# Optimization experiments

Hardware: AMD Instinct MI355X
Metric: run time of the kernel (lower is better)

## Reference

```python
import jax, jax.numpy as jnp
import numpy as np

N = 50000
E = 800000
D = 64
UNITS = 128


def _linear_params(key, fan_in, fan_out):
    k1, k2 = jax.random.split(key)
    bound = 1.0 / np.sqrt(fan_in)
    W = jax.random.uniform(k1, (fan_in, fan_out), minval=-bound, maxval=bound, dtype=jnp.float32)
    b = jax.random.uniform(k2, (fan_out,), minval=-bound, maxval=bound, dtype=jnp.float32)
    return W, b


def setup_inputs() -> dict:
    key = jax.random.key(0)
    ks = jax.random.split(key, 7)
    x = jax.random.normal(ks[0], (N, D), dtype=jnp.float32)
    edge_tensor = jax.random.randint(ks[1], (2, E), 0, N, dtype=jnp.int64)
    W1, b1 = _linear_params(ks[2], D, 2 * D)
    W2, b2 = _linear_params(ks[3], 2 * D, 4 * D)
    W3, b3 = _linear_params(ks[4], 4 * D, UNITS)
    W4, b4 = _linear_params(ks[5], UNITS, UNITS)
    W5, b5 = _linear_params(ks[6], UNITS, 1)
    return {"x": x, "edge_tensor": edge_tensor,
            "W1": W1, "b1": b1, "W2": W2, "b2": b2, "W3": W3, "b3": b3,
            "W4": W4, "b4": b4, "W5": W5, "b5": b5}


def _gin_conv(h, src, dst, W, b):
    # GINConv with default eps=0: MLP((1+eps)*x_i + sum_{j in N(i)} x_j)
    msgs = h[src]                                    # [E, d] gather
    agg = jax.ops.segment_sum(msgs, dst, num_segments=N)  # [N, d] scatter-add
    return jax.nn.relu((agg + h) @ W + b)


def reference(x, edge_tensor, W1, b1, W2, b2, W3, b3, W4, b4, W5, b5):
    src = edge_tensor[0]
    dst = edge_tensor[1]
    h = _gin_conv(x, src, dst, W1, b1)   # [N, 2D]
    h = _gin_conv(h, src, dst, W2, b2)   # [N, 4D]
    h = jax.nn.relu(h @ W3 + b3)         # [N, units]
    h = jax.nn.relu(h @ W4 + b4)         # [N, units]
    return h @ W5 + b5                   # [N, 1]
```

## Files before the change

kernel.cpp:

```cpp
#include <hip/hip_runtime.h>
#include <cstddef>

#define N_NODES 50000
#define N_EDGES 800000

__global__ void zero_int_kernel(int* __restrict__ p, int n) {
    int stride = gridDim.x * blockDim.x;
    for (int i = blockIdx.x * blockDim.x + threadIdx.x; i < n; i += stride) p[i] = 0;
}

__global__ void hist_kernel(const int* __restrict__ dst, int* __restrict__ deg, int E) {
    int stride = gridDim.x * blockDim.x;
    for (int e = blockIdx.x * blockDim.x + threadIdx.x; e < E; e += stride)
        atomicAdd(&deg[dst[e]], 1);
}

__global__ __launch_bounds__(1024)
void scan_blocks(const int* __restrict__ deg, int* __restrict__ loc,
                 int* __restrict__ part, int n) {
    __shared__ int wsum[16];
    const int lane = threadIdx.x & 63;
    const int wid  = threadIdx.x >> 6;
    int i = blockIdx.x * 1024 + threadIdx.x;
    int v = (i < n) ? deg[i] : 0;
    int s = v;
#pragma unroll
    for (int off = 1; off < 64; off <<= 1) {
        int t = __shfl_up(s, off, 64);
        if (lane >= off) s += t;
    }
    if (lane == 63) wsum[wid] = s;
    __syncthreads();
    if (wid == 0) {
        int ws = (lane < 16) ? wsum[lane] : 0;
#pragma unroll
        for (int off = 1; off < 16; off <<= 1) {
            int t = __shfl_up(ws, off, 64);
            if (lane >= off) ws += t;
        }
        if (lane < 16) wsum[lane] = ws;
    }
    __syncthreads();
    int excl = (wid ? wsum[wid - 1] : 0) + s - v;
    if (i < n) loc[i] = excl;
    if (threadIdx.x == 1023) part[blockIdx.x] = wsum[15];
}

__global__ void scan_tops(int* __restrict__ part, int nb) {
    int lane = threadIdx.x;
    int v = (lane < nb) ? part[lane] : 0;
    int s = v;
#pragma unroll
    for (int off = 1; off < 64; off <<= 1) {
        int t = __shfl_up(s, off, 64);
        if (lane >= off) s += t;
    }
    if (lane < nb) part[lane] = s - v;
    if (lane == nb - 1) part[nb] = s;
}

__global__ __launch_bounds__(1024)
void scan_add(const int* __restrict__ loc, const int* __restrict__ part,
              int* __restrict__ row_ptr, int* __restrict__ cursor, int n, int nb) {
    int i = blockIdx.x * 1024 + threadIdx.x;
    if (i < n) {
        int r = loc[i] + part[i >> 10];
        row_ptr[i] = r;
        cursor[i]  = r;
    }
    if (i == 0) row_ptr[n] = part[nb];
}

__global__ void fill_kernel(const int* __restrict__ src, const int* __restrict__ dst,
                            int* __restrict__ cursor, int* __restrict__ col, int E) {
    int stride = gridDim.x * blockDim.x;
    for (int e = blockIdx.x * blockDim.x + threadIdx.x; e < E; e += stride) {
        int p = atomicAdd(&cursor[dst[e]], 1);
        col[p] = src[e];
    }
}

template<int D>
__global__ __launch_bounds__(256)
void gin_aggregate(const float* __restrict__ feat, const int* __restrict__ row_ptr,
                   const int* __restrict__ col, float* __restrict__ agg, int n) {
    int gwid = (blockIdx.x * blockDim.x + threadIdx.x) >> 6;
    int lane = threadIdx.x & 63;
    int nwav = (gridDim.x * blockDim.x) >> 6;
    for (int v = gwid; v < n; v += nwav) {
        float2 acc;
        if constexpr (D == 128) acc = ((const float2*)(feat + (size_t)v * D))[lane];
        else { acc.x = feat[(size_t)v * D + lane]; acc.y = 0.f; }
        int beg = row_ptr[v], end = row_ptr[v + 1];
        for (int j = beg; j < end; j += 64) {
            int batch = end - j; if (batch > 64) batch = 64;
            int e = (lane < batch) ? col[j + lane] : 0;
            for (int k = 0; k < batch; ++k) {
                int s = __shfl(e, k, 64);
                if constexpr (D == 128) {
                    float2 r = ((const float2*)(feat + (size_t)s * D))[lane];
                    acc.x += r.x; acc.y += r.y;
                } else {
                    acc.x += feat[(size_t)s * D + lane];
                }
            }
        }
        if constexpr (D == 128) ((float2*)(agg + (size_t)v * D))[lane] = acc;
        else agg[(size_t)v * D + lane] = acc.x;
    }
}

template<int BN>
__global__ __launch_bounds__(256)
void gemm_bias_relu(const float* __restrict__ A, const float* __restrict__ W,
                    const float* __restrict__ bias, float* __restrict__ C,
                    int M, int K, int N, int do_relu) {
    constexpr int TN = BN / 16;
    __shared__ __align__(16) float As[16][132];
    __shared__ __align__(16) float Bs[16][BN + 4];

    const int tid = threadIdx.x;
    const int tx  = tid & 15;
    const int ty  = tid >> 4;
    const int row0 = blockIdx.y * 128;
    const int col0 = blockIdx.x * BN;

    float acc[8][TN];
#pragma unroll
    for (int i = 0; i < 8; ++i)
#pragma unroll
        for (int j = 0; j < TN; ++j) acc[i][j] = 0.f;

    constexpr int BF4   = BN / 4;
    constexpr int BLOAD = 16 * BF4 / 256;

    for (int k0 = 0; k0 < K; k0 += 16) {
#pragma unroll
        for (int h = 0; h < 2; ++h) {
            int idx = tid + h * 256;
            int ar  = idx >> 2;
            int akc = (idx & 3) << 2;
            int arow = row0 + ar; if (arow >= M) arow = M - 1;
            float4 av = *(const float4*)(A + (size_t)arow * K + k0 + akc);
            As[akc + 0][ar] = av.x;
            As[akc + 1][ar] = av.y;
            As[akc + 2][ar] = av.z;
            As[akc + 3][ar] = av.w;
        }
#pragma unroll
        for (int h = 0; h < BLOAD; ++h) {
            int idx = tid + h * 256;
            int kr  = idx / BF4;
            int cc  = (idx % BF4) << 2;
            float4 bv = *(const float4*)(W + (size_t)(k0 + kr) * N + col0 + cc);
            *(float4*)(&Bs[kr][cc]) = bv;
        }
        __syncthreads();
#pragma unroll
        for (int kk = 0; kk < 16; ++kk) {
            float a[8];
            float4 a0 = *(const float4*)(&As[kk][ty << 2]);
            float4 a1 = *(const float4*)(&As[kk][64 + (ty << 2)]);
            a[0]=a0.x; a[1]=a0.y; a[2]=a0.z; a[3]=a0.w;
            a[4]=a1.x; a[5]=a1.y; a[6]=a1.z; a[7]=a1.w;
            float b[TN];
            float4 b0 = *(const float4*)(&Bs[kk][tx << 2]);
            b[0]=b0.x; b[1]=b0.y; b[2]=b0.z; b[3]=b0.w;
            if constexpr (TN == 8) {
                float4 b1 = *(const float4*)(&Bs[kk][64 + (tx << 2)]);
                b[4]=b1.x; b[5]=b1.y; b[6]=b1.z; b[7]=b1.w;
            }
#pragma unroll
            for (int i = 0; i < 8; ++i)
#pragma unroll
                for (int j = 0; j < TN; ++j)
                    acc[i][j] = fmaf(a[i], b[j], acc[i][j]);
        }
        __syncthreads();
    }

    float bs[TN];
    {
        float4 bb0 = *(const float4*)(bias + col0 + (tx << 2));
        bs[0]=bb0.x; bs[1]=bb0.y; bs[2]=bb0.z; bs[3]=bb0.w;
        if constexpr (TN == 8) {
            float4 bb1 = *(const float4*)(bias + col0 + 64 + (tx << 2));
            bs[4]=bb1.x; bs[5]=bb1.y; bs[6]=bb1.z; bs[7]=bb1.w;
        }
    }
#pragma unroll
    for (int i = 0; i < 8; ++i) {
        int row = row0 + ((i < 4) ? (ty << 2) + i : 64 + (ty << 2) + (i - 4));
        if (row < M) {
#pragma unroll
            for (int g = 0; g < TN / 4; ++g) {
                float4 v;
                float* vp = &v.x;
#pragma unroll
                for (int j = 0; j < 4; ++j) {
                    float t = acc[i][g * 4 + j] + bs[g * 4 + j];
                    if (do_relu) t = fmaxf(t, 0.f);
                    vp[j] = t;
                }
                *(float4*)(C + (size_t)row * N + col0 + g * 64 + (tx << 2)) = v;
            }
        }
    }
}

__global__ void out_proj_kernel(const float* __restrict__ h, const float* __restrict__ w,
                                const float* __restrict__ b, float* __restrict__ out, int M) {
    int lane = threadIdx.x & 63;
    int wave = threadIdx.x >> 6;
    int wpb  = blockDim.x >> 6;
    float w0 = w[lane], w1 = w[64 + lane];
    float bb = b[0];
    for (int row = blockIdx.x * wpb + wave; row < M; row += gridDim.x * wpb) {
        const float* hr = h + (size_t)row * 128;
        float s = hr[lane] * w0 + hr[64 + lane] * w1;
#pragma unroll
        for (int off = 32; off > 0; off >>= 1) s += __shfl_xor(s, off, 64);
        if (lane == 0) out[row] = s + bb;
    }
}

extern "C" void kernel_launch(void* const* d_in, const int* in_sizes, int n_in,
                              void* d_out, int out_size, void* d_ws, size_t ws_size,
                              hipStream_t stream) {
    const float* x    = (const float*)d_in[0];
    const int*   edge = (const int*)d_in[1];
    const float* W1 = (const float*)d_in[2];
    const float* b1 = (const float*)d_in[3];
    const float* W2 = (const float*)d_in[4];
    const float* b2 = (const float*)d_in[5];
    const float* W3 = (const float*)d_in[6];
    const float* b3 = (const float*)d_in[7];
    const float* W4 = (const float*)d_in[8];
    const float* b4 = (const float*)d_in[9];
    const float* W5 = (const float*)d_in[10];
    const float* b5 = (const float*)d_in[11];
    float* out = (float*)d_out;

    const int N = N_NODES, E = N_EDGES;
    const int* src = edge;
    const int* dst = edge + E;

    float* ws   = (float*)d_ws;
    float* h1   = ws;
    float* agg1 = ws + (size_t)N * 128;
    float* agg2 = ws + (size_t)N * 256;
    float* h2   = ws;
    float* h3   = ws + (size_t)N * 256;
    float* h4   = ws;

    int* ibase   = (int*)(ws + (size_t)N * 384);
    int* deg     = ibase;
    int* row_ptr = ibase + N;
    int* colidx  = ibase + 2 * N + 1;
    int* loc     = ibase + 2 * N + 1 + E;
    int* part    = loc + N;

    const int NB = (N + 1023) / 1024;

    dim3 blk(256);

    zero_int_kernel<<<64, blk, 0, stream>>>(deg, N);
    hist_kernel<<<2048, blk, 0, stream>>>(dst, deg, E);
    scan_blocks<<<NB, 1024, 0, stream>>>(deg, loc, part, N);
    scan_tops<<<1, 64, 0, stream>>>(part, NB);
    scan_add<<<NB, 1024, 0, stream>>>(loc, part, row_ptr, deg, N, NB);
    fill_kernel<<<2048, blk, 0, stream>>>(src, dst, deg, colidx, E);

    gin_aggregate<64><<<3125, blk, 0, stream>>>(x, row_ptr, colidx, agg1, N);
    gemm_bias_relu<64><<<dim3(2, 391), blk, 0, stream>>>(agg1, W1, b1, h1, N, 64, 128, 1);

    gin_aggregate<128><<<3125, blk, 0, stream>>>(h1, row_ptr, colidx, agg2, N);
    gemm_bias_relu<128><<<dim3(2, 391), blk, 0, stream>>>(agg2, W2, b2, h2, N, 128, 256, 1);

    gemm_bias_relu<64><<<dim3(2, 391), blk, 0, stream>>>(h2, W3, b3, h3, N, 256, 128, 1);
    gemm_bias_relu<64><<<dim3(2, 391), blk, 0, stream>>>(h3, W4, b4, h4, N, 128, 128, 1);
    out_proj_kernel<<<2048, blk, 0, stream>>>(h4, W5, b5, out, N);
}
```

Measured before the change: 460.9 us.

## Replace FP32 SIMT GEMMs with split-bf16 MFMA GEMMs for the MLP layers

```diff
diff --git a/kernel.cpp b/kernel.cpp
--- a/kernel.cpp
+++ b/kernel.cpp
@@ -1,8 +1,13 @@
 #include <hip/hip_runtime.h>
 #include <cstddef>
+#include <cstdint>
 
 #define N_NODES 50000
 #define N_EDGES 800000
+
+typedef __bf16 bf16x8 __attribute__((ext_vector_type(8)));
+typedef __bf16 bf16x4 __attribute__((ext_vector_type(4)));
+typedef float  f32x4  __attribute__((ext_vector_type(4)));
 
 __global__ void zero_int_kernel(int* __restrict__ p, int n) {
     int stride = gridDim.x * blockDim.x;
@@ -110,99 +115,112 @@
     }
 }
 
-template<int BN>
+__global__ void wsplit_kernel(const float* __restrict__ W, __bf16* __restrict__ Wth,
+                              __bf16* __restrict__ Wtl, int K, int N) {
+    int id = blockIdx.x * blockDim.x + threadIdx.x;
+    if (id >= K * N) return;
+    int k = id / N, n = id % N;
+    float w = W[id];
+    __bf16 h = (__bf16)w;
+    __bf16 l = (__bf16)(w - (float)h);
+    Wth[(size_t)n * K + k] = h;
+    Wtl[(size_t)n * K + k] = l;
+}
+
 __global__ __launch_bounds__(256)
-void gemm_bias_relu(const float* __restrict__ A, const float* __restrict__ W,
-                    const float* __restrict__ bias, float* __restrict__ C,
-                    int M, int K, int N, int do_relu) {
-    constexpr int TN = BN / 16;
-    __shared__ __align__(16) float As[16][132];
-    __shared__ __align__(16) float Bs[16][BN + 4];
-
-    const int tid = threadIdx.x;
-    const int tx  = tid & 15;
-    const int ty  = tid >> 4;
+void gemm_split_bias_relu(const float* __restrict__ A, const __bf16* __restrict__ Wth,
+                          const __bf16* __restrict__ Wtl, const float* __restrict__ bias,
+                          float* __restrict__ C, int M, int K, int N, int do_relu) {
+    __shared__ __align__(16) __bf16 Ah[128][40];
+    __shared__ __align__(16) __bf16 Al[128][40];
+    __shared__ __align__(16) __bf16 Bh[64][40];
+    __shared__ __align__(16) __bf16 Bl[64][40];
+
+    const int tid  = threadIdx.x;
+    const int lane = tid & 63;
+    const int wave = tid >> 6;
+    const int wm   = wave >> 1;
+    const int wn   = wave & 1;
     const int row0 = blockIdx.y * 128;
-    const int col0 = blockIdx.x * BN;
-
-    float acc[8][TN];
-#pragma unroll
-    for (int i = 0; i < 8; ++i)
-#pragma unroll
-        for (int j = 0; j < TN; ++j) acc[i][j] = 0.f;
-
-    constexpr int BF4   = BN / 4;
-    constexpr int BLOAD = 16 * BF4 / 256;
-
-    for (int k0 = 0; k0 < K; k0 += 16) {
-#pragma unroll
-        for (int h = 0; h < 2; ++h) {
-            int idx = tid + h * 256;
-            int ar  = idx >> 2;
-            int akc = (idx & 3) << 2;
-            int arow = row0 + ar; if (arow >= M) arow = M - 1;
-            float4 av = *(const float4*)(A + (size_t)arow * K + k0 + akc);
-            As[akc + 0][ar] = av.x;
-            As[akc + 1][ar] = av.y;
-            As[akc + 2][ar] = av.z;
-            As[akc + 3][ar] = av.w;
-        }
-#pragma unroll
-        for (int h = 0; h < BLOAD; ++h) {
-            int idx = tid + h * 256;
-            int kr  = idx / BF4;
-            int cc  = (idx % BF4) << 2;
-            float4 bv = *(const float4*)(W + (size_t)(k0 + kr) * N + col0 + cc);
-            *(float4*)(&Bs[kr][cc]) = bv;
+    const int col0 = blockIdx.x * 64;
+
+    const int srow = tid >> 1;
+    const int skh  = (tid & 1) * 16;
+    int arow = row0 + srow; if (arow >= M) arow = M - 1;
+    const float* aptr = A + (size_t)arow * K + skh;
+
+    const int bn   = tid >> 2;
+    const int bseg = (tid & 3) * 8;
+    const __bf16* bhptr = Wth + (size_t)(col0 + bn) * K + bseg;
+    const __bf16* blptr = Wtl + (size_t)(col0 + bn) * K + bseg;
+
+    f32x4 acc[4][2];
+#pragma unroll
+    for (int i = 0; i < 4; ++i)
+#pragma unroll
+        for (int j = 0; j < 2; ++j) acc[i][j] = (f32x4){0.f, 0.f, 0.f, 0.f};
+
+    const int g8 = (lane >> 4) * 8;
+    const int fr = lane & 15;
+
+    for (int k0 = 0; k0 < K; k0 += 32) {
+#pragma unroll
+        for (int i = 0; i < 4; ++i) {
+            float4 v = *(const float4*)(aptr + k0 + i * 4);
+            __bf16 h0 = (__bf16)v.x, h1 = (__bf16)v.y, h2 = (__bf16)v.z, h3 = (__bf16)v.w;
+            __bf16 l0 = (__bf16)(v.x - (float)h0);
+            __bf16 l1 = (__bf16)(v.y - (float)h1);
+            __bf16 l2 = (__bf16)(v.z - (float)h2);
+            __bf16 l3 = (__bf16)(v.w - (float)h3);
+            *(bf16x4*)&Ah[srow][skh + i * 4] = (bf16x4){h0, h1, h2, h3};
+            *(bf16x4*)&Al[srow][skh + i * 4] = (bf16x4){l0, l1, l2, l3};
+        }
+        {
+            uint4 hb = *(const uint4*)(bhptr + k0);
+            uint4 lb = *(const uint4*)(blptr + k0);
+            *(uint4*)&Bh[bn][bseg] = hb;
+            *(uint4*)&Bl[bn][bseg] = lb;
         }
         __syncthreads();
-#pragma unroll
-        for (int kk = 0; kk < 16; ++kk) {
-            float a[8];
-            float4 a0 = *(const float4*)(&As[kk][ty << 2]);
-            float4 a1 = *(const float4*)(&As[kk][64 + (ty << 2)]);
-            a[0]=a0.x; a[1]=a0.y; a[2]=a0.z; a[3]=a0.w;
-            a[4]=a1.x; a[5]=a1.y; a[6]=a1.z; a[7]=a1.w;
-            float b[TN];
-            float4 b0 = *(const float4*)(&Bs[kk][tx << 2]);
-            b[0]=b0.x; b[1]=b0.y; b[2]=b0.z; b[3]=b0.w;
-            if constexpr (TN == 8) {
-                float4 b1 = *(const float4*)(&Bs[kk][64 + (tx << 2)]);
-                b[4]=b1.x; b[5]=b1.y; b[6]=b1.z; b[7]=b1.w;
+
+        bf16x8 bh_[2], bl_[2];
+#pragma unroll
+        for (int ni = 0; ni < 2; ++ni) {
+            int n = wn * 32 + ni * 16 + fr;
+            bh_[ni] = *(const bf16x8*)&Bh[n][g8];
+            bl_[ni] = *(const bf16x8*)&Bl[n][g8];
+        }
+#pragma unroll
+        for (int mi = 0; mi < 4; ++mi) {
+            int r = wm * 64 + mi * 16 + fr;
+            bf16x8 ah = *(const bf16x8*)&Ah[r][g8];
+            bf16x8 al = *(const bf16x8*)&Al[r][g8];
+#pragma unroll
+            for (int ni = 0; ni < 2; ++ni) {
+                acc[mi][ni] = __builtin_amdgcn_mfma_f32_16x16x32_bf16(ah, bh_[ni], acc[mi][ni], 0, 0, 0);
+                acc[mi][ni] = __builtin_amdgcn_mfma_f32_16x16x32_bf16(ah, bl_[ni], acc[mi][ni], 0, 0, 0);
+                acc[mi][ni] = __builtin_amdgcn_mfma_f32_16x16x32_bf16(al, bh_[ni], acc[mi][ni], 0, 0, 0);
             }
-#pragma unroll
-            for (int i = 0; i < 8; ++i)
-#pragma unroll
-                for (int j = 0; j < TN; ++j)
-                    acc[i][j] = fmaf(a[i], b[j], acc[i][j]);
         }
         __syncthreads();
     }
 
-    float bs[TN];
-    {
-        float4 bb0 = *(const float4*)(bias + col0 + (tx << 2));
-        bs[0]=bb0.x; bs[1]=bb0.y; bs[2]=bb0.z; bs[3]=bb0.w;
-        if constexpr (TN == 8) {
-            float4 bb1 = *(const float4*)(bias + col0 + 64 + (tx << 2));
-            bs[4]=bb1.x; bs[5]=bb1.y; bs[6]=bb1.z; bs[7]=bb1.w;
-        }
-    }
-#pragma unroll
-    for (int i = 0; i < 8; ++i) {
-        int row = row0 + ((i < 4) ? (ty << 2) + i : 64 + (ty << 2) + (i - 4));
-        if (row < M) {
-#pragma unroll
-            for (int g = 0; g < TN / 4; ++g) {
-                float4 v;
-                float* vp = &v.x;
-#pragma unroll
-                for (int j = 0; j < 4; ++j) {
-                    float t = acc[i][g * 4 + j] + bs[g * 4 + j];
+    const int fq = lane >> 4;
+#pragma unroll
+    for (int ni = 0; ni < 2; ++ni) {
+        int colg = col0 + wn * 32 + ni * 16 + fr;
+        float bc = bias[colg];
+#pragma unroll
+        for (int mi = 0; mi < 4; ++mi) {
+            int rbase = row0 + wm * 64 + mi * 16 + fq * 4;
+#pragma unroll
+            for (int j = 0; j < 4; ++j) {
+                int r = rbase + j;
+                if (r < M) {
+                    float t = acc[mi][ni][j] + bc;
                     if (do_relu) t = fmaxf(t, 0.f);
-                    vp[j] = t;
+                    C[(size_t)r * N + colg] = t;
                 }
-                *(float4*)(C + (size_t)row * N + col0 + g * 64 + (tx << 2)) = v;
             }
         }
     }
@@ -260,9 +278,21 @@
     int* loc     = ibase + 2 * N + 1 + E;
     int* part    = loc + N;
 
+    uintptr_t wp = (uintptr_t)(part + 65);
+    wp = (wp + 15) & ~(uintptr_t)15;
+    __bf16* wtb  = (__bf16*)wp;
+    __bf16* w1h = wtb;            __bf16* w1l = w1h + 64 * 128;
+    __bf16* w2h = w1l + 64 * 128; __bf16* w2l = w2h + 128 * 256;
+    __bf16* w3h = w2l + 128 * 256; __bf16* w3l = w3h + 256 * 128;
+    __bf16* w4h = w3l + 256 * 128; __bf16* w4l = w4h + 128 * 128;
+
     const int NB = (N + 1023) / 1024;
-
     dim3 blk(256);
+
+    wsplit_kernel<<<(64 * 128 + 255) / 256, blk, 0, stream>>>(W1, w1h, w1l, 64, 128);
+    wsplit_kernel<<<(128 * 256 + 255) / 256, blk, 0, stream>>>(W2, w2h, w2l, 128, 256);
+    wsplit_kernel<<<(256 * 128 + 255) / 256, blk, 0, stream>>>(W3, w3h, w3l, 256, 128);
+    wsplit_kernel<<<(128 * 128 + 255) / 256, blk, 0, stream>>>(W4, w4h, w4l, 128, 128);
 
     zero_int_kernel<<<64, blk, 0, stream>>>(deg, N);
     hist_kernel<<<2048, blk, 0, stream>>>(dst, deg, E);
@@ -272,12 +302,12 @@
     fill_kernel<<<2048, blk, 0, stream>>>(src, dst, deg, colidx, E);
 
     gin_aggregate<64><<<3125, blk, 0, stream>>>(x, row_ptr, colidx, agg1, N);
-    gemm_bias_relu<64><<<dim3(2, 391), blk, 0, stream>>>(agg1, W1, b1, h1, N, 64, 128, 1);
+    gemm_split_bias_relu<<<dim3(2, 391), blk, 0, stream>>>(agg1, w1h, w1l, b1, h1, N, 64, 128, 1);
 
     gin_aggregate<128><<<3125, blk, 0, stream>>>(h1, row_ptr, colidx, agg2, N);
-    gemm_bias_relu<128><<<dim3(2, 391), blk, 0, stream>>>(agg2, W2, b2, h2, N, 128, 256, 1);
-
-    gemm_bias_relu<64><<<dim3(2, 391), blk, 0, stream>>>(h2, W3, b3, h3, N, 256, 128, 1);
-    gemm_bias_relu<64><<<dim3(2, 391), blk, 0, stream>>>(h3, W4, b4, h4, N, 128, 128, 1);
+    gemm_split_bias_relu<<<dim3(4, 391), blk, 0, stream>>>(agg2, w2h, w2l, b2, h2, N, 128, 256, 1);
+
+    gemm_split_bias_relu<<<dim3(2, 391), blk, 0, stream>>>(h2, w3h, w3l, b3, h3, N, 256, 128, 1);
+    gemm_split_bias_relu<<<dim3(2, 391), blk, 0, stream>>>(h3, w4h, w4l, b4, h4, N, 128, 128, 1);
     out_proj_kernel<<<2048, blk, 0, stream>>>(h4, W5, b5, out, N);
 }
```

Measured after the change: 417.0 us. 9.5% less time.
